# Performance work log

Hardware: AMD Instinct MI355X
Metric: run time of the kernel (lower is better)

Reference implementation:

```python
import jax, jax.numpy as jnp
import numpy as np

INIT_STDEV = 0.01

def setup_inputs() -> dict:
    key = jax.random.key(0)
    k1, k2, k3 = jax.random.split(key, 3)
    B, S, D = 8, 4096, 768
    x = jax.random.normal(k1, (B, S, D), dtype=jnp.float32)
    att_v = jax.random.normal(k2, (D,), dtype=jnp.float32) * INIT_STDEV
    att_W = jax.random.normal(k3, (D, D), dtype=jnp.float32) * INIT_STDEV
    return {"x": x, "att_v": att_v, "att_W": att_W}

def reference(x, att_v, att_W):
    # y = x @ W : [B,S,D]; scores = tanh(y) . v over D : [B,S]
    y = jnp.tanh(jnp.einsum('bsd,de->bse', x, att_W))
    scores = jnp.einsum('bsd,d->bs', y, att_v)
    weights = jax.nn.softmax(scores, axis=-1)            # softmax over sequence
    out = jnp.einsum('bs,bsd->bd', weights, x)           # attsum pool
    return out.astype(jnp.float32)
```

## Files before the change

kernel.cpp:

```cpp
#include <hip/hip_runtime.h>
#include <hip/hip_bf16.h>

constexpr int Bb = 8;
constexpr int Ss = 4096;
constexpr int Dd = 768;
constexpr int Mm = Bb * Ss;

typedef __bf16 bf16x8 __attribute__((ext_vector_type(8)));
typedef __bf16 bf16x4 __attribute__((ext_vector_type(4)));
typedef float f32x4 __attribute__((ext_vector_type(4)));

__device__ __forceinline__ float fast_tanh(float x) {
    return 1.f - 2.f / (__expf(2.f * x) + 1.f);
}

__device__ __forceinline__ void load_lds16(const void* g, void* l) {
    __builtin_amdgcn_global_load_lds(
        (const __attribute__((address_space(1))) unsigned int*)g,
        (__attribute__((address_space(3))) unsigned int*)l, 16, 0, 0);
}

__global__ __launch_bounds__(256) void convW(const float* __restrict__ W,
                                             __bf16* __restrict__ Wt) {
    __shared__ float tile[32][33];
    const int tx = threadIdx.x & 31;
    const int ty = threadIdx.x >> 5;
    const int kb = blockIdx.x * 32;
    const int nb = blockIdx.y * 32;
#pragma unroll
    for (int i = 0; i < 32; i += 8)
        tile[ty + i][tx] = W[(size_t)(kb + ty + i) * Dd + nb + tx];
    __syncthreads();
#pragma unroll
    for (int i = 0; i < 32; i += 8) {
        const int n = nb + ty + i;
        const int txs = (tx & 7) | ((((tx >> 3) & 3) ^ ((n >> 1) & 3)) << 3);
        Wt[(size_t)n * Dd + kb + txs] = (__bf16)tile[tx][ty + i];
    }
}

__global__ __launch_bounds__(512, 4) void scores_gemm(
    const float* __restrict__ x, const __bf16* __restrict__ Wt,
    const float* __restrict__ v, float* __restrict__ scores) {
    __shared__ __bf16 As[2][128 * 32];
    __shared__ __bf16 Bs[2][256 * 32];
    __shared__ float ssc[8][64];

    const int t = threadIdx.x;
    const int nb = blockIdx.x;
    const int mb = blockIdx.y;
    const int lane = t & 63;
    const int wave = t >> 6;
    const int wm = wave >> 2;
    const int wn = wave & 3;
    const int quad = lane >> 4;
    const int lid = lane & 15;
    const int rslot = ((quad ^ ((lid >> 1) & 3)) * 8);

    const int arow = t >> 2;
    const int aslotraw = t & 3;
    const int aslot = aslotraw ^ ((arow >> 1) & 3);
    const float* agp = x + (size_t)(mb * 128 + arow) * Dd + aslotraw * 8;
    const int awr = arow * 32 + aslot * 8;

    const __bf16* bg[2];
    int bl[2];
#pragma unroll
    for (int j = 0; j < 2; ++j) {
        const int flat = j * 8192 + t * 16;
        const int col = flat >> 6;
        bg[j] = Wt + (size_t)(nb * 256 + col) * Dd + ((flat & 63) >> 1);
        bl[j] = flat >> 1;
    }

    f32x4 acc[4][4];
#pragma unroll
    for (int tm = 0; tm < 4; ++tm)
#pragma unroll
        for (int nt = 0; nt < 4; ++nt) acc[tm][nt] = (f32x4){0.f, 0.f, 0.f, 0.f};

    {
        const float4 a0 = *(const float4*)(agp);
        const float4 a1 = *(const float4*)(agp + 4);
        bf16x8 pa;
        pa[0] = (__bf16)a0.x; pa[1] = (__bf16)a0.y; pa[2] = (__bf16)a0.z; pa[3] = (__bf16)a0.w;
        pa[4] = (__bf16)a1.x; pa[5] = (__bf16)a1.y; pa[6] = (__bf16)a1.z; pa[7] = (__bf16)a1.w;
        *(bf16x8*)(&As[0][awr]) = pa;
#pragma unroll
        for (int j = 0; j < 2; ++j) load_lds16(bg[j], &Bs[0][bl[j]]);
    }

    for (int kb = 0; kb < 24; ++kb) {
        const int p = kb & 1;
        __syncthreads();

        float4 a0n, a1n;
        if (kb < 23) {
            a0n = *(const float4*)(agp + (kb + 1) * 32);
            a1n = *(const float4*)(agp + (kb + 1) * 32 + 4);
#pragma unroll
            for (int j = 0; j < 2; ++j)
                load_lds16(bg[j] + (kb + 1) * 32, &Bs[1 - p][bl[j]]);
        }

        bf16x8 af[4], bfr[4];
#pragma unroll
        for (int tm = 0; tm < 4; ++tm)
            af[tm] = *(const bf16x8*)(&As[p][(wm * 64 + tm * 16 + lid) * 32 + rslot]);
#pragma unroll
        for (int nt = 0; nt < 4; ++nt)
            bfr[nt] = *(const bf16x8*)(&Bs[p][(wn * 64 + nt * 16 + lid) * 32 + rslot]);

#pragma unroll
        for (int tm = 0; tm < 4; ++tm)
#pragma unroll
            for (int nt = 0; nt < 4; ++nt)
                acc[tm][nt] = __builtin_amdgcn_mfma_f32_16x16x32_bf16(af[tm], bfr[nt], acc[tm][nt], 0, 0, 0);

        if (kb < 23) {
            bf16x8 pa;
            pa[0] = (__bf16)a0n.x; pa[1] = (__bf16)a0n.y; pa[2] = (__bf16)a0n.z; pa[3] = (__bf16)a0n.w;
            pa[4] = (__bf16)a1n.x; pa[5] = (__bf16)a1n.y; pa[6] = (__bf16)a1n.z; pa[7] = (__bf16)a1n.w;
            *(bf16x8*)(&As[1 - p][awr]) = pa;
        }
    }

    float vv[4];
#pragma unroll
    for (int nt = 0; nt < 4; ++nt)
        vv[nt] = v[nb * 256 + wn * 64 + nt * 16 + lid];

#pragma unroll
    for (int tm = 0; tm < 4; ++tm)
#pragma unroll
        for (int r = 0; r < 4; ++r) {
            float s = 0.f;
#pragma unroll
            for (int nt = 0; nt < 4; ++nt) s += vv[nt] * fast_tanh(acc[tm][nt][r]);
            s += __shfl_xor(s, 1);
            s += __shfl_xor(s, 2);
            s += __shfl_xor(s, 4);
            s += __shfl_xor(s, 8);
            if (lid == 0) ssc[wave][tm * 16 + quad * 4 + r] = s;
        }
    __syncthreads();
    if (t < 128) {
        const int wmh = t >> 6;
        const int rl = t & 63;
        float s = 0.f;
#pragma unroll
        for (int ww = 0; ww < 4; ++ww) s += ssc[wmh * 4 + ww][rl];
        atomicAdd(&scores[mb * 128 + t], s);
    }
}

__global__ __launch_bounds__(256) void softmax_k(const float* __restrict__ scores,
                                                 float* __restrict__ weights) {
    const int b = blockIdx.x;
    const int t = threadIdx.x;
    const float* s = scores + (size_t)b * Ss;
    float* wgt = weights + (size_t)b * Ss;
    __shared__ float red[256];

    float mx = -1e30f;
    for (int i = t; i < Ss; i += 256) mx = fmaxf(mx, s[i]);
    red[t] = mx;
    __syncthreads();
    for (int o = 128; o > 0; o >>= 1) {
        if (t < o) red[t] = fmaxf(red[t], red[t + o]);
        __syncthreads();
    }
    mx = red[0];
    __syncthreads();
    float sum = 0.f;
    for (int i = t; i < Ss; i += 256) {
        const float e = __expf(s[i] - mx);
        wgt[i] = e;
        sum += e;
    }
    red[t] = sum;
    __syncthreads();
    for (int o = 128; o > 0; o >>= 1) {
        if (t < o) red[t] += red[t + o];
        __syncthreads();
    }
    const float inv = 1.f / red[0];
    for (int i = t; i < Ss; i += 256) wgt[i] *= inv;
}

__global__ __launch_bounds__(192) void pool1(const float* __restrict__ x,
                                             const float* __restrict__ weights,
                                             float* __restrict__ partial) {
    const int b = blockIdx.y;
    const int c = blockIdx.x;
    const int t = threadIdx.x;
    const float* base = x + ((size_t)b * Ss + c * 32) * Dd;
    const float* wrow = weights + (size_t)b * Ss + c * 32;
    float4 acc = make_float4(0.f, 0.f, 0.f, 0.f);
#pragma unroll 8
    for (int i = 0; i < 32; ++i) {
        const float ww = wrow[i];
        const float4 xv = *(const float4*)(base + (size_t)i * Dd + t * 4);
        acc.x += ww * xv.x;
        acc.y += ww * xv.y;
        acc.z += ww * xv.z;
        acc.w += ww * xv.w;
    }
    *(float4*)(partial + ((size_t)(b * 128 + c)) * Dd + t * 4) = acc;
}

__global__ __launch_bounds__(768) void pool2(const float* __restrict__ partial,
                                             float* __restrict__ out) {
    const int b = blockIdx.x;
    const int d = threadIdx.x;
    float s = 0.f;
#pragma unroll 8
    for (int c = 0; c < 128; ++c) s += partial[((size_t)(b * 128 + c)) * Dd + d];
    out[(size_t)b * Dd + d] = s;
}

extern "C" void kernel_launch(void* const* d_in, const int* in_sizes, int n_in,
                              void* d_out, int out_size, void* d_ws, size_t ws_size,
                              hipStream_t stream) {
    (void)in_sizes; (void)n_in; (void)ws_size; (void)out_size;
    const float* x = (const float*)d_in[0];
    const float* v = (const float*)d_in[1];
    const float* W = (const float*)d_in[2];

    char* ws = (char*)d_ws;
    __bf16* Wt = (__bf16*)ws;
    float* scores = (float*)(ws + 1179648);
    float* weights = (float*)(ws + 1179648 + 131072);
    float* partial = (float*)(ws + 1179648 + 262144);

    hipMemsetAsync(scores, 0, Mm * sizeof(float), stream);

    convW<<<dim3(Dd / 32, Dd / 32), 256, 0, stream>>>(W, Wt);
    scores_gemm<<<dim3(3, Mm / 128), 512, 0, stream>>>(x, Wt, v, scores);
    softmax_k<<<dim3(Bb), 256, 0, stream>>>(scores, weights);
    pool1<<<dim3(128, Bb), 192, 0, stream>>>(x, weights, partial);
    pool2<<<dim3(Bb), 768, 0, stream>>>(partial, (float*)d_out);
}
```

Before: 238.9 us.

## Triple-buffer GEMM B tiles, remap blocks, drop score atomics and pool2 kernel

The scores GEMM moves to a three-stage LDS ring for the W tiles, with explicit waitcnt and barrier placement plus raised priority around the MFMAs. A 1D grid is remapped so that the 8 XCD slots each get contiguous M blocks. Per-N-block scores are written to three separate buffers instead of using atomics, which removes the memset on scores. Softmax no longer normalizes the weights and instead stores 1/sum, which pool1 applies before atomically accumulating into the output, so the pool2 kernel is dropped. The trade is more LDS use, which may lower occupancy, plus float atomics in pool1 whose summation order is not deterministic.

```diff
diff --git a/kernel.cpp b/kernel.cpp
--- a/kernel.cpp
+++ b/kernel.cpp
@@ -41,14 +41,16 @@
 
 __global__ __launch_bounds__(512, 4) void scores_gemm(
     const float* __restrict__ x, const __bf16* __restrict__ Wt,
-    const float* __restrict__ v, float* __restrict__ scores) {
-    __shared__ __bf16 As[2][128 * 32];
-    __shared__ __bf16 Bs[2][256 * 32];
+    const float* __restrict__ v, float* __restrict__ scores3) {
+    __shared__ __bf16 As[3][128 * 32];
+    __shared__ __bf16 Bs[3][256 * 32];
     __shared__ float ssc[8][64];
 
     const int t = threadIdx.x;
-    const int nb = blockIdx.x;
-    const int mb = blockIdx.y;
+    const int id = blockIdx.x;
+    const int ids = ((id & 7) * 96) + (id >> 3);
+    const int mb = ids / 3;
+    const int nb = ids - mb * 3;
     const int lane = t & 63;
     const int wave = t >> 6;
     const int wm = wave >> 2;
@@ -80,48 +82,59 @@
         for (int nt = 0; nt < 4; ++nt) acc[tm][nt] = (f32x4){0.f, 0.f, 0.f, 0.f};
 
     {
-        const float4 a0 = *(const float4*)(agp);
-        const float4 a1 = *(const float4*)(agp + 4);
-        bf16x8 pa;
-        pa[0] = (__bf16)a0.x; pa[1] = (__bf16)a0.y; pa[2] = (__bf16)a0.z; pa[3] = (__bf16)a0.w;
-        pa[4] = (__bf16)a1.x; pa[5] = (__bf16)a1.y; pa[6] = (__bf16)a1.z; pa[7] = (__bf16)a1.w;
-        *(bf16x8*)(&As[0][awr]) = pa;
+        const float4 pa0 = *(const float4*)(agp);
+        const float4 pa1 = *(const float4*)(agp + 4);
 #pragma unroll
         for (int j = 0; j < 2; ++j) load_lds16(bg[j], &Bs[0][bl[j]]);
-    }
-
-    for (int kb = 0; kb < 24; ++kb) {
-        const int p = kb & 1;
-        __syncthreads();
+#pragma unroll
+        for (int j = 0; j < 2; ++j) load_lds16(bg[j] + 32, &Bs[1][bl[j]]);
+        bf16x8 w;
+        w[0] = (__bf16)pa0.x; w[1] = (__bf16)pa0.y; w[2] = (__bf16)pa0.z; w[3] = (__bf16)pa0.w;
+        w[4] = (__bf16)pa1.x; w[5] = (__bf16)pa1.y; w[6] = (__bf16)pa1.z; w[7] = (__bf16)pa1.w;
+        *(bf16x8*)(&As[0][awr]) = w;
+    }
+
+#pragma unroll
+    for (int k = 0; k < 24; ++k) {
+        if (k == 23) asm volatile("s_waitcnt vmcnt(0) lgkmcnt(0)" ::: "memory");
+        else         asm volatile("s_waitcnt vmcnt(2) lgkmcnt(0)" ::: "memory");
+        __builtin_amdgcn_sched_barrier(0);
+        __builtin_amdgcn_s_barrier();
+        __builtin_amdgcn_sched_barrier(0);
 
         float4 a0n, a1n;
-        if (kb < 23) {
-            a0n = *(const float4*)(agp + (kb + 1) * 32);
-            a1n = *(const float4*)(agp + (kb + 1) * 32 + 4);
+        if (k < 23) {
+            a0n = *(const float4*)(agp + (k + 1) * 32);
+            a1n = *(const float4*)(agp + (k + 1) * 32 + 4);
+        }
+        __builtin_amdgcn_sched_barrier(0);
+        if (k < 22) {
 #pragma unroll
             for (int j = 0; j < 2; ++j)
-                load_lds16(bg[j] + (kb + 1) * 32, &Bs[1 - p][bl[j]]);
+                load_lds16(bg[j] + (k + 2) * 32, &Bs[(k + 2) % 3][bl[j]]);
         }
 
         bf16x8 af[4], bfr[4];
 #pragma unroll
         for (int tm = 0; tm < 4; ++tm)
-            af[tm] = *(const bf16x8*)(&As[p][(wm * 64 + tm * 16 + lid) * 32 + rslot]);
+            af[tm] = *(const bf16x8*)(&As[k % 3][(wm * 64 + tm * 16 + lid) * 32 + rslot]);
 #pragma unroll
         for (int nt = 0; nt < 4; ++nt)
-            bfr[nt] = *(const bf16x8*)(&Bs[p][(wn * 64 + nt * 16 + lid) * 32 + rslot]);
-
+            bfr[nt] = *(const bf16x8*)(&Bs[k % 3][(wn * 64 + nt * 16 + lid) * 32 + rslot]);
+
+        __builtin_amdgcn_s_setprio(1);
 #pragma unroll
         for (int tm = 0; tm < 4; ++tm)
 #pragma unroll
             for (int nt = 0; nt < 4; ++nt)
                 acc[tm][nt] = __builtin_amdgcn_mfma_f32_16x16x32_bf16(af[tm], bfr[nt], acc[tm][nt], 0, 0, 0);
-
-        if (kb < 23) {
+        __builtin_amdgcn_s_setprio(0);
+
+        if (k < 23) {
             bf16x8 pa;
             pa[0] = (__bf16)a0n.x; pa[1] = (__bf16)a0n.y; pa[2] = (__bf16)a0n.z; pa[3] = (__bf16)a0n.w;
             pa[4] = (__bf16)a1n.x; pa[5] = (__bf16)a1n.y; pa[6] = (__bf16)a1n.z; pa[7] = (__bf16)a1n.w;
-            *(bf16x8*)(&As[1 - p][awr]) = pa;
+            *(bf16x8*)(&As[(k + 1) % 3][awr]) = pa;
         }
     }
 
@@ -150,20 +163,27 @@
         float s = 0.f;
 #pragma unroll
         for (int ww = 0; ww < 4; ++ww) s += ssc[wmh * 4 + ww][rl];
-        atomicAdd(&scores[mb * 128 + t], s);
-    }
-}
-
-__global__ __launch_bounds__(256) void softmax_k(const float* __restrict__ scores,
-                                                 float* __restrict__ weights) {
+        scores3[(size_t)nb * Mm + mb * 128 + t] = s;
+    }
+}
+
+__global__ __launch_bounds__(256) void softmax_k(const float* __restrict__ scores3,
+                                                 float* __restrict__ weights,
+                                                 float* __restrict__ sinv) {
     const int b = blockIdx.x;
     const int t = threadIdx.x;
-    const float* s = scores + (size_t)b * Ss;
+    const float* s0 = scores3 + (size_t)b * Ss;
+    const float* s1 = s0 + Mm;
+    const float* s2 = s1 + Mm;
     float* wgt = weights + (size_t)b * Ss;
     __shared__ float red[256];
 
     float mx = -1e30f;
-    for (int i = t; i < Ss; i += 256) mx = fmaxf(mx, s[i]);
+    for (int i = t; i < Ss; i += 256) {
+        const float sc = s0[i] + s1[i] + s2[i];
+        wgt[i] = sc;
+        mx = fmaxf(mx, sc);
+    }
     red[t] = mx;
     __syncthreads();
     for (int o = 128; o > 0; o >>= 1) {
@@ -174,7 +194,7 @@
     __syncthreads();
     float sum = 0.f;
     for (int i = t; i < Ss; i += 256) {
-        const float e = __expf(s[i] - mx);
+        const float e = __expf(wgt[i] - mx);
         wgt[i] = e;
         sum += e;
     }
@@ -184,13 +204,13 @@
         if (t < o) red[t] += red[t + o];
         __syncthreads();
     }
-    const float inv = 1.f / red[0];
-    for (int i = t; i < Ss; i += 256) wgt[i] *= inv;
+    if (t == 0) sinv[b] = 1.f / red[0];
 }
 
 __global__ __launch_bounds__(192) void pool1(const float* __restrict__ x,
                                              const float* __restrict__ weights,
-                                             float* __restrict__ partial) {
+                                             const float* __restrict__ sinv,
+                                             float* __restrict__ out) {
     const int b = blockIdx.y;
     const int c = blockIdx.x;
     const int t = threadIdx.x;
@@ -206,17 +226,12 @@
         acc.z += ww * xv.z;
         acc.w += ww * xv.w;
     }
-    *(float4*)(partial + ((size_t)(b * 128 + c)) * Dd + t * 4) = acc;
-}
-
-__global__ __launch_bounds__(768) void pool2(const float* __restrict__ partial,
-                                             float* __restrict__ out) {
-    const int b = blockIdx.x;
-    const int d = threadIdx.x;
-    float s = 0.f;
-#pragma unroll 8
-    for (int c = 0; c < 128; ++c) s += partial[((size_t)(b * 128 + c)) * Dd + d];
-    out[(size_t)b * Dd + d] = s;
+    const float inv = sinv[b];
+    float* o = out + (size_t)b * Dd + t * 4;
+    atomicAdd(o + 0, acc.x * inv);
+    atomicAdd(o + 1, acc.y * inv);
+    atomicAdd(o + 2, acc.z * inv);
+    atomicAdd(o + 3, acc.w * inv);
 }
 
 extern "C" void kernel_launch(void* const* d_in, const int* in_sizes, int n_in,
@@ -229,15 +244,14 @@
 
     char* ws = (char*)d_ws;
     __bf16* Wt = (__bf16*)ws;
-    float* scores = (float*)(ws + 1179648);
-    float* weights = (float*)(ws + 1179648 + 131072);
-    float* partial = (float*)(ws + 1179648 + 262144);
-
-    hipMemsetAsync(scores, 0, Mm * sizeof(float), stream);
+    float* scores3 = (float*)(ws + 1179648);
+    float* weights = (float*)(ws + 1179648 + 393216);
+    float* sinv    = (float*)(ws + 1179648 + 393216 + 131072);
+
+    hipMemsetAsync(d_out, 0, Bb * Dd * sizeof(float), stream);
 
     convW<<<dim3(Dd / 32, Dd / 32), 256, 0, stream>>>(W, Wt);
-    scores_gemm<<<dim3(3, Mm / 128), 512, 0, stream>>>(x, Wt, v, scores);
-    softmax_k<<<dim3(Bb), 256, 0, stream>>>(scores, weights);
-    pool1<<<dim3(128, Bb), 192, 0, stream>>>(x, weights, partial);
-    pool2<<<dim3(Bb), 768, 0, stream>>>(partial, (float*)d_out);
-}
+    scores_gemm<<<dim3(3 * Mm / 128), 512, 0, stream>>>(x, Wt, v, scores3);
+    softmax_k<<<dim3(Bb), 256, 0, stream>>>(scores3, weights, sinv);
+    pool1<<<dim3(128, Bb), 192, 0, stream>>>(x, weights, sinv, (float*)d_out);
+}
```

Result: no change. 242.7 us (+1.6%).
